# Kernel tuning notes

Hardware: AMD Instinct MI355X
Metric: run time of the kernel (lower is better)

Reference implementation:

```python
import jax, jax.numpy as jnp
import numpy as np

N_NODES = 100000
N_EDGES = 1600000
IN_F = 64
H1_F = 64
N_CLS = 16
NEG_SLOPE = 0.01  # F.leaky_relu default


def _sage_pool(x, src, dst, n_nodes, W_pool, b_pool, W_self, W_neigh, bias):
    """DGL SAGEConv with aggregator_type='pool'.
    msg = relu(x[src] @ W_pool + b_pool); pooled = max over in-edges per dst
    out = x @ W_self + pooled @ W_neigh + bias (empty segments pooled to 0)."""
    m = jax.nn.relu(x[src] @ W_pool + b_pool)                 # [E, d_in]
    pooled = jax.ops.segment_max(m, dst, num_segments=n_nodes)  # [N, d_in]
    deg = jax.ops.segment_sum(jnp.ones(dst.shape[0], x.dtype), dst,
                              num_segments=n_nodes)           # [N]
    pooled = jnp.where(deg[:, None] > 0, pooled, jnp.zeros((), x.dtype))
    return x @ W_self + pooled @ W_neigh + bias               # [N, d_out]


def setup_inputs() -> dict:
    key = jax.random.key(0)
    ks = jax.random.split(key, 12)
    sc_in = 1.0 / np.sqrt(IN_F)
    sc_h1 = 1.0 / np.sqrt(H1_F)
    inp = {
        "in_feat": jax.random.normal(ks[0], (N_NODES, IN_F), jnp.float32),
        "src": jax.random.randint(ks[1], (N_EDGES,), 0, N_NODES),
        "dst": jax.random.randint(ks[2], (N_EDGES,), 0, N_NODES),
        # layer 1 (in=64 -> out=64)
        "W_pool1": jax.random.normal(ks[3], (IN_F, IN_F), jnp.float32) * sc_in,
        "b_pool1": jnp.zeros((IN_F,), jnp.float32),
        "W_self1": jax.random.normal(ks[4], (IN_F, H1_F), jnp.float32) * sc_in,
        "W_neigh1": jax.random.normal(ks[5], (IN_F, H1_F), jnp.float32) * sc_in,
        "bias1": jnp.zeros((H1_F,), jnp.float32),
        # layer 2 (in=64 -> out=16)
        "W_pool2": jax.random.normal(ks[6], (H1_F, H1_F), jnp.float32) * sc_h1,
        "b_pool2": jnp.zeros((H1_F,), jnp.float32),
        "W_self2": jax.random.normal(ks[7], (H1_F, N_CLS), jnp.float32) * sc_h1,
        "W_neigh2": jax.random.normal(ks[8], (H1_F, N_CLS), jnp.float32) * sc_h1,
        "bias2": jnp.zeros((N_CLS,), jnp.float32),
    }
    return inp


def reference(in_feat, src, dst,
              W_pool1, b_pool1, W_self1, W_neigh1, bias1,
              W_pool2, b_pool2, W_self2, W_neigh2, bias2):
    n = in_feat.shape[0]
    h = _sage_pool(in_feat, src, dst, n, W_pool1, b_pool1, W_self1, W_neigh1, bias1)
    h = jnp.where(h >= 0, h, NEG_SLOPE * h)  # leaky_relu
    out = _sage_pool(h, src, dst, n, W_pool2, b_pool2, W_self2, W_neigh2, bias2)
    return out
```

## Files before the change

### kernel.cpp

```cpp
#include <hip/hip_runtime.h>
#include <cstddef>
#include <cstdint>

#define CAP 64
#define SCAP 40
#define CHUNK2 4096
#define PR 5120

typedef _Float16 h2 __attribute__((ext_vector_type(2)));
static __device__ __forceinline__ h2 h2max(h2 a, h2 b) {
  return __builtin_elementwise_max(a, b);
}
static __device__ __forceinline__ h2 bch2(int u) { return __builtin_bit_cast(h2, u); }
static __device__ __forceinline__ int packrelu(float a, float b) {
  h2 t; t.x = (_Float16)fmaxf(a, 0.f); t.y = (_Float16)fmaxf(b, 0.f);
  return __builtin_bit_cast(int, t);
}
static __device__ __forceinline__ int packleaky(float a, float b) {
  float la = (a >= 0.f) ? a : 0.01f * a;
  float lb = (b >= 0.f) ? b : 0.01f * b;
  h2 t; t.x = (_Float16)la; t.y = (_Float16)lb;
  return __builtin_bit_cast(int, t);
}
static __device__ __forceinline__ float fdot2f(h2 a, h2 b, float c) {
#if __has_builtin(__builtin_amdgcn_fdot2)
  return __builtin_amdgcn_fdot2(a, b, c, false);
#else
  return c + (float)a.x * (float)b.x + (float)a.y * (float)b.y;
#endif
}

__global__ __launch_bounds__(256) void k_binscatter(const int* __restrict__ src,
                                                    const int* __restrict__ dst,
                                                    unsigned int* __restrict__ pairs,
                                                    int* __restrict__ cnt2,
                                                    int E, int P) {
  __shared__ int hcnt[512];
  int tid = threadIdx.x;
  for (int p = tid; p < 512; p += 256) hcnt[p] = 0;
  __syncthreads();
  int chunk = blockIdx.x;
  int e0 = chunk * CHUNK2;
  unsigned int* pbase = pairs + (size_t)chunk * P * SCAP;
  #pragma unroll
  for (int k = 0; k < CHUNK2 / 256; k++) {
    int e = e0 + k * 256 + tid;
    if (e < E) {
      int d = dst[e], s = src[e];
      int p = d >> 8;
      int slot = atomicAdd(&hcnt[p], 1);
      if (slot < SCAP)
        pbase[p * SCAP + slot] = (unsigned)s | ((unsigned)(d & 255) << 17);
    }
  }
  __syncthreads();
  int* cbase = cnt2 + (size_t)chunk * P;
  for (int p = tid; p < P; p += 256) {
    int c = hcnt[p];
    cbase[p] = (c < SCAP) ? c : SCAP;
  }
}

__global__ __launch_bounds__(256) void k_fill3(const unsigned int* __restrict__ pairs,
                                               const int* __restrict__ cnt2,
                                               int* __restrict__ cnt,
                                               int* __restrict__ rowstart,
                                               int* __restrict__ bucket,
                                               int n, int NC, int P) {
  __shared__ int sbucket[256 * CAP];
  __shared__ int scnt[256];
  __shared__ int soff[256];
  __shared__ int scnt2[512];
  int tid = threadIdx.x;
  int p = blockIdx.x;
  scnt[tid] = 0;
  for (int c = tid; c < NC; c += 256) scnt2[c] = cnt2[(size_t)c * P + p];
  __syncthreads();
  int total = NC * SCAP;
  for (int t = tid; t < total; t += 256) {
    int chunk = t / SCAP;
    int slot = t - chunk * SCAP;
    if (slot < scnt2[chunk]) {
      unsigned int u = pairs[(size_t)chunk * P * SCAP + p * SCAP + slot];
      int s = (int)(u & 0x1FFFFu);
      int dlow = (int)(u >> 17);
      int sl = atomicAdd(&scnt[dlow], 1);
      if (sl < CAP)
        sbucket[dlow * CAP + sl] = s;
    }
  }
  __syncthreads();
  int c = scnt[tid];
  if (c > CAP) c = CAP;
  int ca = (c + 3) & ~3;
  soff[tid] = ca;
  __syncthreads();
  #pragma unroll
  for (int off = 1; off < 256; off <<= 1) {
    int t = (tid >= off) ? soff[tid - off] : 0;
    __syncthreads();
    soff[tid] += t;
    __syncthreads();
  }
  int local = soff[tid] - ca;
  int node = (p << 8) + tid;
  int gbase = p * PR + local;
  if (node < n) {
    cnt[node] = c;
    rowstart[node] = gbase;
  }
  for (int j = 0; j < c; j += 4) {
    int4 v = *(const int4*)&sbucket[tid * CAP + j];
    *(int4*)&bucket[gbase + j] = v;
  }
}

__global__ __launch_bounds__(256) void k_z(const float* __restrict__ X,
                                           const float* __restrict__ W,
                                           const float* __restrict__ bias,
                                           _Float16* __restrict__ Z, int n) {
  __shared__ __attribute__((aligned(16))) h2 sW[32 * 64];
  __shared__ __attribute__((aligned(16))) h2 sXT[32 * 128];
  int tid = threadIdx.x;
  #pragma unroll
  for (int it = 0; it < 8; it++) {
    int idx = it * 256 + tid;
    int kp = idx >> 6, c = idx & 63;
    h2 t;
    t.x = (_Float16)W[(2 * kp) * 64 + c];
    t.y = (_Float16)W[(2 * kp + 1) * 64 + c];
    sW[kp * 64 + c] = t;
  }
  int node0 = blockIdx.x * 128;
  #pragma unroll
  for (int it = 0; it < 8; it++) {
    int idx = it * 256 + tid;
    int row = idx & 127, c4 = idx >> 7;
    int node = node0 + row;
    float4 v = make_float4(0.f, 0.f, 0.f, 0.f);
    if (node < n) v = ((const float4*)(X + (size_t)node * 64))[c4];
    h2 a; a.x = (_Float16)v.x; a.y = (_Float16)v.y;
    h2 d; d.x = (_Float16)v.z; d.y = (_Float16)v.w;
    sXT[(2 * c4 + 0) * 128 + row] = a;
    sXT[(2 * c4 + 1) * 128 + row] = d;
  }
  __syncthreads();
  int lane = tid & 63;
  int cg = tid >> 6;
  float acc0[16], acc1[16];
  #pragma unroll
  for (int c4 = 0; c4 < 4; c4++) {
    float4 bv = ((const float4*)bias)[cg * 4 + c4];
    acc0[c4 * 4 + 0] = bv.x; acc0[c4 * 4 + 1] = bv.y;
    acc0[c4 * 4 + 2] = bv.z; acc0[c4 * 4 + 3] = bv.w;
    acc1[c4 * 4 + 0] = bv.x; acc1[c4 * 4 + 1] = bv.y;
    acc1[c4 * 4 + 2] = bv.z; acc1[c4 * 4 + 3] = bv.w;
  }
  #pragma unroll 8
  for (int kp = 0; kp < 32; kp++) {
    h2 x0 = sXT[kp * 128 + lane];
    h2 x1 = sXT[kp * 128 + lane + 64];
    const int4* wq = (const int4*)(sW + kp * 64 + cg * 16);
    #pragma unroll
    for (int q4 = 0; q4 < 4; q4++) {
      int4 wv = wq[q4];
      h2 w0 = bch2(wv.x), w1 = bch2(wv.y), w2 = bch2(wv.z), w3 = bch2(wv.w);
      acc0[q4 * 4 + 0] = fdot2f(x0, w0, acc0[q4 * 4 + 0]);
      acc0[q4 * 4 + 1] = fdot2f(x0, w1, acc0[q4 * 4 + 1]);
      acc0[q4 * 4 + 2] = fdot2f(x0, w2, acc0[q4 * 4 + 2]);
      acc0[q4 * 4 + 3] = fdot2f(x0, w3, acc0[q4 * 4 + 3]);
      acc1[q4 * 4 + 0] = fdot2f(x1, w0, acc1[q4 * 4 + 0]);
      acc1[q4 * 4 + 1] = fdot2f(x1, w1, acc1[q4 * 4 + 1]);
      acc1[q4 * 4 + 2] = fdot2f(x1, w2, acc1[q4 * 4 + 2]);
      acc1[q4 * 4 + 3] = fdot2f(x1, w3, acc1[q4 * 4 + 3]);
    }
  }
  int nodeA = node0 + lane;
  int nodeB = node0 + lane + 64;
  if (nodeA < n) {
    int4 o0, o1;
    o0.x = packrelu(acc0[0], acc0[1]);   o0.y = packrelu(acc0[2], acc0[3]);
    o0.z = packrelu(acc0[4], acc0[5]);   o0.w = packrelu(acc0[6], acc0[7]);
    o1.x = packrelu(acc0[8], acc0[9]);   o1.y = packrelu(acc0[10], acc0[11]);
    o1.z = packrelu(acc0[12], acc0[13]); o1.w = packrelu(acc0[14], acc0[15]);
    char* rp = (char*)Z + (size_t)nodeA * 128 + cg * 32;
    ((int4*)rp)[0] = o0; ((int4*)rp)[1] = o1;
  }
  if (nodeB < n) {
    int4 o0, o1;
    o0.x = packrelu(acc1[0], acc1[1]);   o0.y = packrelu(acc1[2], acc1[3]);
    o0.z = packrelu(acc1[4], acc1[5]);   o0.w = packrelu(acc1[6], acc1[7]);
    o1.x = packrelu(acc1[8], acc1[9]);   o1.y = packrelu(acc1[10], acc1[11]);
    o1.z = packrelu(acc1[12], acc1[13]); o1.w = packrelu(acc1[14], acc1[15]);
    char* rp = (char*)Z + (size_t)nodeB * 128 + cg * 32;
    ((int4*)rp)[0] = o0; ((int4*)rp)[1] = o1;
  }
}

__global__ __launch_bounds__(256) void k_hl(const float* __restrict__ X,
                                            const _Float16* __restrict__ P,
                                            const float* __restrict__ Ws,
                                            const float* __restrict__ Wn,
                                            const float* __restrict__ bias,
                                            const float* __restrict__ Wp2,
                                            const float* __restrict__ bp2,
                                            _Float16* __restrict__ H,
                                            _Float16* __restrict__ Z2, int n) {
  __shared__ __attribute__((aligned(16))) h2 sWs[32 * 64];
  __shared__ __attribute__((aligned(16))) h2 sWn[32 * 64];
  __shared__ __attribute__((aligned(16))) h2 sXT[32 * 128];
  __shared__ __attribute__((aligned(16))) h2 sPT[32 * 128];
  int tid = threadIdx.x;
  #pragma unroll
  for (int it = 0; it < 8; it++) {
    int idx = it * 256 + tid;
    int kp = idx >> 6, c = idx & 63;
    h2 t1, t2;
    t1.x = (_Float16)Ws[(2 * kp) * 64 + c];
    t1.y = (_Float16)Ws[(2 * kp + 1) * 64 + c];
    t2.x = (_Float16)Wn[(2 * kp) * 64 + c];
    t2.y = (_Float16)Wn[(2 * kp + 1) * 64 + c];
    sWs[kp * 64 + c] = t1;
    sWn[kp * 64 + c] = t2;
  }
  int node0 = blockIdx.x * 128;
  #pragma unroll
  for (int it = 0; it < 8; it++) {
    int idx = it * 256 + tid;
    int row = idx & 127, c4 = idx >> 7;
    int node = node0 + row;
    float4 v = make_float4(0.f, 0.f, 0.f, 0.f);
    if (node < n) v = ((const float4*)(X + (size_t)node * 64))[c4];
    h2 a; a.x = (_Float16)v.x; a.y = (_Float16)v.y;
    h2 d; d.x = (_Float16)v.z; d.y = (_Float16)v.w;
    sXT[(2 * c4 + 0) * 128 + row] = a;
    sXT[(2 * c4 + 1) * 128 + row] = d;
  }
  #pragma unroll
  for (int it = 0; it < 4; it++) {
    int idx = it * 256 + tid;
    int row = idx & 127, q = idx >> 7;
    int node = node0 + row;
    int4 u = make_int4(0, 0, 0, 0);
    if (node < n) u = ((const int4*)((const char*)P + (size_t)node * 128))[q];
    sPT[(4 * q + 0) * 128 + row] = bch2(u.x);
    sPT[(4 * q + 1) * 128 + row] = bch2(u.y);
    sPT[(4 * q + 2) * 128 + row] = bch2(u.z);
    sPT[(4 * q + 3) * 128 + row] = bch2(u.w);
  }
  __syncthreads();
  int lane = tid & 63;
  int cg = tid >> 6;
  float acc0[16], acc1[16];
  #pragma unroll
  for (int c4 = 0; c4 < 4; c4++) {
    float4 bv = ((const float4*)bias)[cg * 4 + c4];
    acc0[c4 * 4 + 0] = bv.x; acc0[c4 * 4 + 1] = bv.y;
    acc0[c4 * 4 + 2] = bv.z; acc0[c4 * 4 + 3] = bv.w;
    acc1[c4 * 4 + 0] = bv.x; acc1[c4 * 4 + 1] = bv.y;
    acc1[c4 * 4 + 2] = bv.z; acc1[c4 * 4 + 3] = bv.w;
  }
  #pragma unroll 8
  for (int kp = 0; kp < 32; kp++) {
    h2 x0 = sXT[kp * 128 + lane];
    h2 x1 = sXT[kp * 128 + lane + 64];
    h2 p0 = sPT[kp * 128 + lane];
    h2 p1 = sPT[kp * 128 + lane + 64];
    const int4* wsq = (const int4*)(sWs + kp * 64 + cg * 16);
    const int4* wnq = (const int4*)(sWn + kp * 64 + cg * 16);
    #pragma unroll
    for (int q4 = 0; q4 < 4; q4++) {
      int4 a = wsq[q4];
      int4 d = wnq[q4];
      h2 s0 = bch2(a.x), s1 = bch2(a.y), s2 = bch2(a.z), s3 = bch2(a.w);
      h2 n0 = bch2(d.x), n1 = bch2(d.y), n2 = bch2(d.z), n3 = bch2(d.w);
      acc0[q4 * 4 + 0] = fdot2f(x0, s0, acc0[q4 * 4 + 0]);
      acc0[q4 * 4 + 1] = fdot2f(x0, s1, acc0[q4 * 4 + 1]);
      acc0[q4 * 4 + 2] = fdot2f(x0, s2, acc0[q4 * 4 + 2]);
      acc0[q4 * 4 + 3] = fdot2f(x0, s3, acc0[q4 * 4 + 3]);
      acc0[q4 * 4 + 0] = fdot2f(p0, n0, acc0[q4 * 4 + 0]);
      acc0[q4 * 4 + 1] = fdot2f(p0, n1, acc0[q4 * 4 + 1]);
      acc0[q4 * 4 + 2] = fdot2f(p0, n2, acc0[q4 * 4 + 2]);
      acc0[q4 * 4 + 3] = fdot2f(p0, n3, acc0[q4 * 4 + 3]);
      acc1[q4 * 4 + 0] = fdot2f(x1, s0, acc1[q4 * 4 + 0]);
      acc1[q4 * 4 + 1] = fdot2f(x1, s1, acc1[q4 * 4 + 1]);
      acc1[q4 * 4 + 2] = fdot2f(x1, s2, acc1[q4 * 4 + 2]);
      acc1[q4 * 4 + 3] = fdot2f(x1, s3, acc1[q4 * 4 + 3]);
      acc1[q4 * 4 + 0] = fdot2f(p1, n0, acc1[q4 * 4 + 0]);
      acc1[q4 * 4 + 1] = fdot2f(p1, n1, acc1[q4 * 4 + 1]);
      acc1[q4 * 4 + 2] = fdot2f(p1, n2, acc1[q4 * 4 + 2]);
      acc1[q4 * 4 + 3] = fdot2f(p1, n3, acc1[q4 * 4 + 3]);
    }
  }
  int ha[8], hb[8];
  #pragma unroll
  for (int j = 0; j < 8; j++) {
    ha[j] = packleaky(acc0[2 * j], acc0[2 * j + 1]);
    hb[j] = packleaky(acc1[2 * j], acc1[2 * j + 1]);
  }
  int nodeA = node0 + lane;
  int nodeB = node0 + lane + 64;
  __syncthreads();
  #pragma unroll
  for (int j = 0; j < 8; j++) {
    sXT[(cg * 8 + j) * 128 + lane]      = bch2(ha[j]);
    sXT[(cg * 8 + j) * 128 + lane + 64] = bch2(hb[j]);
  }
  #pragma unroll
  for (int it = 0; it < 8; it++) {
    int idx = it * 256 + tid;
    int kp = idx >> 6, c = idx & 63;
    h2 t;
    t.x = (_Float16)Wp2[(2 * kp) * 64 + c];
    t.y = (_Float16)Wp2[(2 * kp + 1) * 64 + c];
    sWs[kp * 64 + c] = t;
  }
  if (nodeA < n) {
    char* rp = (char*)H + (size_t)nodeA * 128 + cg * 32;
    ((int4*)rp)[0] = make_int4(ha[0], ha[1], ha[2], ha[3]);
    ((int4*)rp)[1] = make_int4(ha[4], ha[5], ha[6], ha[7]);
  }
  if (nodeB < n) {
    char* rp = (char*)H + (size_t)nodeB * 128 + cg * 32;
    ((int4*)rp)[0] = make_int4(hb[0], hb[1], hb[2], hb[3]);
    ((int4*)rp)[1] = make_int4(hb[4], hb[5], hb[6], hb[7]);
  }
  __syncthreads();
  float c0[16], c1[16];
  #pragma unroll
  for (int c4 = 0; c4 < 4; c4++) {
    float4 bv = ((const float4*)bp2)[cg * 4 + c4];
    c0[c4 * 4 + 0] = bv.x; c0[c4 * 4 + 1] = bv.y;
    c0[c4 * 4 + 2] = bv.z; c0[c4 * 4 + 3] = bv.w;
    c1[c4 * 4 + 0] = bv.x; c1[c4 * 4 + 1] = bv.y;
    c1[c4 * 4 + 2] = bv.z; c1[c4 * 4 + 3] = bv.w;
  }
  #pragma unroll 8
  for (int kp = 0; kp < 32; kp++) {
    h2 x0 = sXT[kp * 128 + lane];
    h2 x1 = sXT[kp * 128 + lane + 64];
    const int4* wq = (const int4*)(sWs + kp * 64 + cg * 16);
    #pragma unroll
    for (int q4 = 0; q4 < 4; q4++) {
      int4 wv = wq[q4];
      h2 w0 = bch2(wv.x), w1 = bch2(wv.y), w2 = bch2(wv.z), w3 = bch2(wv.w);
      c0[q4 * 4 + 0] = fdot2f(x0, w0, c0[q4 * 4 + 0]);
      c0[q4 * 4 + 1] = fdot2f(x0, w1, c0[q4 * 4 + 1]);
      c0[q4 * 4 + 2] = fdot2f(x0, w2, c0[q4 * 4 + 2]);
      c0[q4 * 4 + 3] = fdot2f(x0, w3, c0[q4 * 4 + 3]);
      c1[q4 * 4 + 0] = fdot2f(x1, w0, c1[q4 * 4 + 0]);
      c1[q4 * 4 + 1] = fdot2f(x1, w1, c1[q4 * 4 + 1]);
      c1[q4 * 4 + 2] = fdot2f(x1, w2, c1[q4 * 4 + 2]);
      c1[q4 * 4 + 3] = fdot2f(x1, w3, c1[q4 * 4 + 3]);
    }
  }
  if (nodeA < n) {
    int4 o0, o1;
    o0.x = packrelu(c0[0], c0[1]);   o0.y = packrelu(c0[2], c0[3]);
    o0.z = packrelu(c0[4], c0[5]);   o0.w = packrelu(c0[6], c0[7]);
    o1.x = packrelu(c0[8], c0[9]);   o1.y = packrelu(c0[10], c0[11]);
    o1.z = packrelu(c0[12], c0[13]); o1.w = packrelu(c0[14], c0[15]);
    char* rp = (char*)Z2 + (size_t)nodeA * 128 + cg * 32;
    ((int4*)rp)[0] = o0; ((int4*)rp)[1] = o1;
  }
  if (nodeB < n) {
    int4 o0, o1;
    o0.x = packrelu(c1[0], c1[1]);   o0.y = packrelu(c1[2], c1[3]);
    o0.z = packrelu(c1[4], c1[5]);   o0.w = packrelu(c1[6], c1[7]);
    o1.x = packrelu(c1[8], c1[9]);   o1.y = packrelu(c1[10], c1[11]);
    o1.z = packrelu(c1[12], c1[13]); o1.w = packrelu(c1[14], c1[15]);
    char* rp = (char*)Z2 + (size_t)nodeB * 128 + cg * 32;
    ((int4*)rp)[0] = o0; ((int4*)rp)[1] = o1;
  }
}

__global__ __launch_bounds__(256) void k_gather(const _Float16* __restrict__ Z,
                                                const int* __restrict__ bucket,
                                                const int* __restrict__ rowstart,
                                                const int* __restrict__ cnt,
                                                _Float16* __restrict__ pooled, int n) {
  int t = blockIdx.x * 256 + threadIdx.x;
  int node = t >> 5;
  int sub = t & 31;
  if (node >= n) return;
  int c = cnt[node];
  const int* bk = bucket + rowstart[node];
  const char* zb = (const char*)Z + sub * 4;
  h2 acc = (h2)(_Float16)0;
  int j = 0;
  for (; j + 8 <= c; j += 8) {
    int4 a = *(const int4*)(bk + j);
    int4 d = *(const int4*)(bk + j + 4);
    int u0 = *(const int*)(zb + (size_t)a.x * 128);
    int u1 = *(const int*)(zb + (size_t)a.y * 128);
    int u2 = *(const int*)(zb + (size_t)a.z * 128);
    int u3 = *(const int*)(zb + (size_t)a.w * 128);
    int u4 = *(const int*)(zb + (size_t)d.x * 128);
    int u5 = *(const int*)(zb + (size_t)d.y * 128);
    int u6 = *(const int*)(zb + (size_t)d.z * 128);
    int u7 = *(const int*)(zb + (size_t)d.w * 128);
    h2 m0 = h2max(bch2(u0), bch2(u1));
    h2 m1 = h2max(bch2(u2), bch2(u3));
    h2 m2 = h2max(bch2(u4), bch2(u5));
    h2 m3 = h2max(bch2(u6), bch2(u7));
    acc = h2max(acc, h2max(h2max(m0, m1), h2max(m2, m3)));
  }
  if (j + 4 <= c) {
    int4 a = *(const int4*)(bk + j);
    int u0 = *(const int*)(zb + (size_t)a.x * 128);
    int u1 = *(const int*)(zb + (size_t)a.y * 128);
    int u2 = *(const int*)(zb + (size_t)a.z * 128);
    int u3 = *(const int*)(zb + (size_t)a.w * 128);
    acc = h2max(acc, h2max(h2max(bch2(u0), bch2(u1)), h2max(bch2(u2), bch2(u3))));
    j += 4;
  }
  if (j + 2 <= c) {
    int2 a = *(const int2*)(bk + j);
    int u0 = *(const int*)(zb + (size_t)a.x * 128);
    int u1 = *(const int*)(zb + (size_t)a.y * 128);
    acc = h2max(acc, h2max(bch2(u0), bch2(u1)));
    j += 2;
  }
  if (j < c) {
    int u0 = *(const int*)(zb + (size_t)bk[j] * 128);
    acc = h2max(acc, bch2(u0));
  }
  *(int*)((char*)pooled + (size_t)node * 128 + sub * 4) = __builtin_bit_cast(int, acc);
}

__global__ __launch_bounds__(256) void k_gather_out(const _Float16* __restrict__ Z,
                                                    const int* __restrict__ bucket,
                                                    const int* __restrict__ rowstart,
                                                    const int* __restrict__ cnt,
                                                    const _Float16* __restrict__ Hrow,
                                                    const float* __restrict__ Ws,
                                                    const float* __restrict__ Wn,
                                                    const float* __restrict__ bias,
                                                    float* __restrict__ OUT, int n) {
  __shared__ __attribute__((aligned(16))) h2 sWs[32 * 16];
  __shared__ __attribute__((aligned(16))) h2 sWn[32 * 16];
  __shared__ __attribute__((aligned(16))) h2 sH[8][32];
  __shared__ __attribute__((aligned(16))) h2 sP[8][32];
  __shared__ float sB[16];
  int tid = threadIdx.x;
  #pragma unroll
  for (int it = 0; it < 2; it++) {
    int idx = it * 256 + tid;
    int kp = idx >> 4, c = idx & 15;
    h2 t1, t2;
    t1.x = (_Float16)Ws[(2 * kp) * 16 + c];
    t1.y = (_Float16)Ws[(2 * kp + 1) * 16 + c];
    t2.x = (_Float16)Wn[(2 * kp) * 16 + c];
    t2.y = (_Float16)Wn[(2 * kp + 1) * 16 + c];
    sWs[kp * 16 + c] = t1;
    sWn[kp * 16 + c] = t2;
  }
  if (tid < 16) sB[tid] = bias[tid];
  int nodeBase = blockIdx.x * 8;
  if (tid < 64) {
    int nd = nodeBase + (tid >> 3);
    int q = tid & 7;
    int4 u = make_int4(0, 0, 0, 0);
    if (nd < n) u = ((const int4*)((const char*)Hrow + (size_t)nd * 128))[q];
    ((int4*)&sH[tid >> 3][0])[q] = u;
  }
  int en = tid >> 5;
  int node = nodeBase + en;
  int sub = tid & 31;
  h2 acc = (h2)(_Float16)0;
  if (node < n) {
    int c = cnt[node];
    const int* bk = bucket + rowstart[node];
    const char* zb = (const char*)Z + sub * 4;
    int j = 0;
    for (; j + 8 <= c; j += 8) {
      int4 a = *(const int4*)(bk + j);
      int4 d = *(const int4*)(bk + j + 4);
      int u0 = *(const int*)(zb + (size_t)a.x * 128);
      int u1 = *(const int*)(zb + (size_t)a.y * 128);
      int u2 = *(const int*)(zb + (size_t)a.z * 128);
      int u3 = *(const int*)(zb + (size_t)a.w * 128);
      int u4 = *(const int*)(zb + (size_t)d.x * 128);
      int u5 = *(const int*)(zb + (size_t)d.y * 128);
      int u6 = *(const int*)(zb + (size_t)d.z * 128);
      int u7 = *(const int*)(zb + (size_t)d.w * 128);
      h2 m0 = h2max(bch2(u0), bch2(u1));
      h2 m1 = h2max(bch2(u2), bch2(u3));
      h2 m2 = h2max(bch2(u4), bch2(u5));
      h2 m3 = h2max(bch2(u6), bch2(u7));
      acc = h2max(acc, h2max(h2max(m0, m1), h2max(m2, m3)));
    }
    if (j + 4 <= c) {
      int4 a = *(const int4*)(bk + j);
      int u0 = *(const int*)(zb + (size_t)a.x * 128);
      int u1 = *(const int*)(zb + (size_t)a.y * 128);
      int u2 = *(const int*)(zb + (size_t)a.z * 128);
      int u3 = *(const int*)(zb + (size_t)a.w * 128);
      acc = h2max(acc, h2max(h2max(bch2(u0), bch2(u1)), h2max(bch2(u2), bch2(u3))));
      j += 4;
    }
    if (j + 2 <= c) {
      int2 a = *(const int2*)(bk + j);
      int u0 = *(const int*)(zb + (size_t)a.x * 128);
      int u1 = *(const int*)(zb + (size_t)a.y * 128);
      acc = h2max(acc, h2max(bch2(u0), bch2(u1)));
      j += 2;
    }
    if (j < c) {
      int u0 = *(const int*)(zb + (size_t)bk[j] * 128);
      acc = h2max(acc, bch2(u0));
    }
  }
  sP[en][sub] = acc;
  __syncthreads();
  int col = tid & 15;
  int kh = (tid >> 4) & 1;
  float v = 0.f;
  #pragma unroll
  for (int j = 0; j < 16; j++) {
    int kp = kh * 16 + j;
    v = fdot2f(sH[en][kp], sWs[kp * 16 + col], v);
    v = fdot2f(sP[en][kp], sWn[kp * 16 + col], v);
  }
  v += __shfl_xor(v, 16);
  if (kh == 0 && node < n)
    OUT[(size_t)node * 16 + col] = v + sB[col];
}

extern "C" void kernel_launch(void* const* d_in, const int* in_sizes, int n_in,
                              void* d_out, int out_size, void* d_ws, size_t ws_size,
                              hipStream_t stream) {
  const float* X   = (const float*)d_in[0];
  const int*   src = (const int*)d_in[1];
  const int*   dst = (const int*)d_in[2];
  const float* Wp1 = (const float*)d_in[3];
  const float* bp1 = (const float*)d_in[4];
  const float* Ws1 = (const float*)d_in[5];
  const float* Wn1 = (const float*)d_in[6];
  const float* b1  = (const float*)d_in[7];
  const float* Wp2 = (const float*)d_in[8];
  const float* bp2 = (const float*)d_in[9];
  const float* Ws2 = (const float*)d_in[10];
  const float* Wn2 = (const float*)d_in[11];
  const float* b2  = (const float*)d_in[12];
  float* OUT = (float*)d_out;

  const int n = in_sizes[0] / 64;
  const int E = in_sizes[1];
  const int P = (n + 255) >> 8;
  const int NC = (E + CHUNK2 - 1) / CHUNK2;

  char* w = (char*)d_ws;
  auto alloc = [&](size_t bytes) -> char* {
    char* p = w;
    w += (bytes + 255) & ~(size_t)255;
    return p;
  };
  int*  cnt      = (int*)alloc((size_t)n * 4);
  int*  rowstart = (int*)alloc((size_t)n * 4);
  int*  bucket   = (int*)alloc((size_t)P * PR * 4);
  int*  cnt2     = (int*)alloc((size_t)NC * P * 4);
  size_t pairs_b = (size_t)NC * P * SCAP * 4;
  size_t h_b     = (size_t)n * 64 * 2;
  char* ali = alloc(pairs_b > h_b ? pairs_b : h_b);
  unsigned int* pairs = (unsigned int*)ali;
  _Float16*     h16   = (_Float16*)ali;
  _Float16* zh     = (_Float16*)alloc((size_t)n * 64 * 2);
  _Float16* pooled = (_Float16*)alloc((size_t)n * 64 * 2);
  (void)ws_size; (void)n_in; (void)out_size;

  const int nbT  = (n + 127) / 128;
  const int nbG  = (n * 32 + 255) / 256;
  const int nbG8 = (n + 7) / 8;

  k_binscatter<<<NC, 256, 0, stream>>>(src, dst, pairs, cnt2, E, P);
  k_fill3<<<P, 256, 0, stream>>>(pairs, cnt2, cnt, rowstart, bucket, n, NC, P);

  k_z<<<nbT, 256, 0, stream>>>(X, Wp1, bp1, zh, n);
  k_gather<<<nbG, 256, 0, stream>>>(zh, bucket, rowstart, cnt, pooled, n);
  k_hl<<<nbT, 256, 0, stream>>>(X, pooled, Ws1, Wn1, b1, Wp2, bp2, h16, zh, n);
  k_gather_out<<<nbG8, 256, 0, stream>>>(zh, bucket, rowstart, cnt, h16,
                                         Ws2, Wn2, b2, OUT, n);
}
```

Before: 190.5 us.

## Merge binscatter with Z projection and pack row count into offset

The edge bin-scatter and the layer-1 pool projection now run as one launch, with the block index choosing the role, so the two independent stages overlap and one launch is saved. Row start and degree are packed into a single int, so each gather reads one index word instead of two. The layer-1 gather now handles two nodes per 32-lane group to give each thread more memory-level parallelism. PR is enlarged to leave room for the packed offset, at the cost of a larger bucket buffer and a 10-bit count field.

Result: faster. 180.4 us (-5.3%).

```diff
diff --git a/kernel.cpp b/kernel.cpp
--- a/kernel.cpp
+++ b/kernel.cpp
@@ -5,7 +5,7 @@
 #define CAP 64
 #define SCAP 40
 #define CHUNK2 4096
-#define PR 5120
+#define PR 5632
 
 typedef _Float16 h2 __attribute__((ext_vector_type(2)));
 static __device__ __forceinline__ h2 h2max(h2 a, h2 b) {
@@ -30,98 +30,45 @@
 #endif
 }
 
-__global__ __launch_bounds__(256) void k_binscatter(const int* __restrict__ src,
-                                                    const int* __restrict__ dst,
-                                                    unsigned int* __restrict__ pairs,
-                                                    int* __restrict__ cnt2,
-                                                    int E, int P) {
-  __shared__ int hcnt[512];
+__global__ __launch_bounds__(256) void k_build(const int* __restrict__ src,
+                                               const int* __restrict__ dst,
+                                               unsigned int* __restrict__ pairs,
+                                               int* __restrict__ cnt2,
+                                               int E, int P, int NC,
+                                               const float* __restrict__ X,
+                                               const float* __restrict__ W,
+                                               const float* __restrict__ bias,
+                                               _Float16* __restrict__ Z, int n) {
+  __shared__ __attribute__((aligned(16))) char smem[24576];
   int tid = threadIdx.x;
-  for (int p = tid; p < 512; p += 256) hcnt[p] = 0;
-  __syncthreads();
-  int chunk = blockIdx.x;
-  int e0 = chunk * CHUNK2;
-  unsigned int* pbase = pairs + (size_t)chunk * P * SCAP;
-  #pragma unroll
-  for (int k = 0; k < CHUNK2 / 256; k++) {
-    int e = e0 + k * 256 + tid;
-    if (e < E) {
-      int d = dst[e], s = src[e];
-      int p = d >> 8;
-      int slot = atomicAdd(&hcnt[p], 1);
-      if (slot < SCAP)
-        pbase[p * SCAP + slot] = (unsigned)s | ((unsigned)(d & 255) << 17);
+  if ((int)blockIdx.x < NC) {
+    int* hcnt = (int*)smem;
+    for (int p = tid; p < 512; p += 256) hcnt[p] = 0;
+    __syncthreads();
+    int chunk = blockIdx.x;
+    int e0 = chunk * CHUNK2;
+    unsigned int* pbase = pairs + (size_t)chunk * P * SCAP;
+    #pragma unroll
+    for (int k = 0; k < CHUNK2 / 256; k++) {
+      int e = e0 + k * 256 + tid;
+      if (e < E) {
+        int d = dst[e], s = src[e];
+        int p = d >> 8;
+        int slot = atomicAdd(&hcnt[p], 1);
+        if (slot < SCAP)
+          pbase[p * SCAP + slot] = (unsigned)s | ((unsigned)(d & 255) << 17);
+      }
     }
-  }
-  __syncthreads();
-  int* cbase = cnt2 + (size_t)chunk * P;
-  for (int p = tid; p < P; p += 256) {
-    int c = hcnt[p];
-    cbase[p] = (c < SCAP) ? c : SCAP;
-  }
-}
-
-__global__ __launch_bounds__(256) void k_fill3(const unsigned int* __restrict__ pairs,
-                                               const int* __restrict__ cnt2,
-                                               int* __restrict__ cnt,
-                                               int* __restrict__ rowstart,
-                                               int* __restrict__ bucket,
-                                               int n, int NC, int P) {
-  __shared__ int sbucket[256 * CAP];
-  __shared__ int scnt[256];
-  __shared__ int soff[256];
-  __shared__ int scnt2[512];
-  int tid = threadIdx.x;
-  int p = blockIdx.x;
-  scnt[tid] = 0;
-  for (int c = tid; c < NC; c += 256) scnt2[c] = cnt2[(size_t)c * P + p];
-  __syncthreads();
-  int total = NC * SCAP;
-  for (int t = tid; t < total; t += 256) {
-    int chunk = t / SCAP;
-    int slot = t - chunk * SCAP;
-    if (slot < scnt2[chunk]) {
-      unsigned int u = pairs[(size_t)chunk * P * SCAP + p * SCAP + slot];
-      int s = (int)(u & 0x1FFFFu);
-      int dlow = (int)(u >> 17);
-      int sl = atomicAdd(&scnt[dlow], 1);
-      if (sl < CAP)
-        sbucket[dlow * CAP + sl] = s;
+    __syncthreads();
+    int* cbase = cnt2 + (size_t)chunk * P;
+    for (int p = tid; p < P; p += 256) {
+      int c = hcnt[p];
+      cbase[p] = (c < SCAP) ? c : SCAP;
     }
-  }
-  __syncthreads();
-  int c = scnt[tid];
-  if (c > CAP) c = CAP;
-  int ca = (c + 3) & ~3;
-  soff[tid] = ca;
-  __syncthreads();
-  #pragma unroll
-  for (int off = 1; off < 256; off <<= 1) {
-    int t = (tid >= off) ? soff[tid - off] : 0;
-    __syncthreads();
-    soff[tid] += t;
-    __syncthreads();
-  }
-  int local = soff[tid] - ca;
-  int node = (p << 8) + tid;
-  int gbase = p * PR + local;
-  if (node < n) {
-    cnt[node] = c;
-    rowstart[node] = gbase;
-  }
-  for (int j = 0; j < c; j += 4) {
-    int4 v = *(const int4*)&sbucket[tid * CAP + j];
-    *(int4*)&bucket[gbase + j] = v;
-  }
-}
-
-__global__ __launch_bounds__(256) void k_z(const float* __restrict__ X,
-                                           const float* __restrict__ W,
-                                           const float* __restrict__ bias,
-                                           _Float16* __restrict__ Z, int n) {
-  __shared__ __attribute__((aligned(16))) h2 sW[32 * 64];
-  __shared__ __attribute__((aligned(16))) h2 sXT[32 * 128];
-  int tid = threadIdx.x;
+    return;
+  }
+  h2* sW  = (h2*)smem;
+  h2* sXT = (h2*)(smem + 8192);
   #pragma unroll
   for (int it = 0; it < 8; it++) {
     int idx = it * 256 + tid;
@@ -131,7 +78,7 @@
     t.y = (_Float16)W[(2 * kp + 1) * 64 + c];
     sW[kp * 64 + c] = t;
   }
-  int node0 = blockIdx.x * 128;
+  int node0 = (blockIdx.x - NC) * 128;
   #pragma unroll
   for (int it = 0; it < 8; it++) {
     int idx = it * 256 + tid;
@@ -194,6 +141,129 @@
     o1.z = packrelu(acc1[12], acc1[13]); o1.w = packrelu(acc1[14], acc1[15]);
     char* rp = (char*)Z + (size_t)nodeB * 128 + cg * 32;
     ((int4*)rp)[0] = o0; ((int4*)rp)[1] = o1;
+  }
+}
+
+__global__ __launch_bounds__(256) void k_fill3(const unsigned int* __restrict__ pairs,
+                                               const int* __restrict__ cnt2,
+                                               int* __restrict__ rowcnt,
+                                               int* __restrict__ bucket,
+                                               int n, int NC, int P) {
+  __shared__ int sbucket[256 * CAP];
+  __shared__ int scnt[256];
+  __shared__ int soff[256];
+  __shared__ int scnt2[512];
+  int tid = threadIdx.x;
+  int p = blockIdx.x;
+  scnt[tid] = 0;
+  for (int c = tid; c < NC; c += 256) scnt2[c] = cnt2[(size_t)c * P + p];
+  __syncthreads();
+  int total = NC * SCAP;
+  for (int t = tid; t < total; t += 256) {
+    int chunk = t / SCAP;
+    int slot = t - chunk * SCAP;
+    if (slot < scnt2[chunk]) {
+      unsigned int u = pairs[(size_t)chunk * P * SCAP + p * SCAP + slot];
+      int s = (int)(u & 0x1FFFFu);
+      int dlow = (int)(u >> 17);
+      int sl = atomicAdd(&scnt[dlow], 1);
+      if (sl < CAP)
+        sbucket[dlow * CAP + sl] = s;
+    }
+  }
+  __syncthreads();
+  int c = scnt[tid];
+  if (c > CAP) c = CAP;
+  int ca = (c + 3) & ~3;
+  soff[tid] = ca;
+  __syncthreads();
+  #pragma unroll
+  for (int off = 1; off < 256; off <<= 1) {
+    int t = (tid >= off) ? soff[tid - off] : 0;
+    __syncthreads();
+    soff[tid] += t;
+    __syncthreads();
+  }
+  int local = soff[tid] - ca;
+  int node = (p << 8) + tid;
+  int gbase = p * PR + local;
+  if (node < n)
+    rowcnt[node] = gbase | (c << 22);
+  for (int j = 0; j < c; j += 4) {
+    int4 v = *(const int4*)&sbucket[tid * CAP + j];
+    *(int4*)&bucket[gbase + j] = v;
+  }
+}
+
+static __device__ __forceinline__ h2 gather_one(const char* zb,
+                                                const int* __restrict__ bucket,
+                                                int rc) {
+  int c = rc >> 22;
+  const int* bk = bucket + (rc & 0x3FFFFF);
+  h2 acc = (h2)(_Float16)0;
+  int j = 0;
+  for (; j + 8 <= c; j += 8) {
+    int4 a = *(const int4*)(bk + j);
+    int4 d = *(const int4*)(bk + j + 4);
+    int u0 = *(const int*)(zb + (size_t)a.x * 128);
+    int u1 = *(const int*)(zb + (size_t)a.y * 128);
+    int u2 = *(const int*)(zb + (size_t)a.z * 128);
+    int u3 = *(const int*)(zb + (size_t)a.w * 128);
+    int u4 = *(const int*)(zb + (size_t)d.x * 128);
+    int u5 = *(const int*)(zb + (size_t)d.y * 128);
+    int u6 = *(const int*)(zb + (size_t)d.z * 128);
+    int u7 = *(const int*)(zb + (size_t)d.w * 128);
+    h2 m0 = h2max(bch2(u0), bch2(u1));
+    h2 m1 = h2max(bch2(u2), bch2(u3));
+    h2 m2 = h2max(bch2(u4), bch2(u5));
+    h2 m3 = h2max(bch2(u6), bch2(u7));
+    acc = h2max(acc, h2max(h2max(m0, m1), h2max(m2, m3)));
+  }
+  if (j + 4 <= c) {
+    int4 a = *(const int4*)(bk + j);
+    int u0 = *(const int*)(zb + (size_t)a.x * 128);
+    int u1 = *(const int*)(zb + (size_t)a.y * 128);
+    int u2 = *(const int*)(zb + (size_t)a.z * 128);
+    int u3 = *(const int*)(zb + (size_t)a.w * 128);
+    acc = h2max(acc, h2max(h2max(bch2(u0), bch2(u1)), h2max(bch2(u2), bch2(u3))));
+    j += 4;
+  }
+  if (j + 2 <= c) {
+    int2 a = *(const int2*)(bk + j);
+    int u0 = *(const int*)(zb + (size_t)a.x * 128);
+    int u1 = *(const int*)(zb + (size_t)a.y * 128);
+    acc = h2max(acc, h2max(bch2(u0), bch2(u1)));
+    j += 2;
+  }
+  if (j < c) {
+    int u0 = *(const int*)(zb + (size_t)bk[j] * 128);
+    acc = h2max(acc, bch2(u0));
+  }
+  return acc;
+}
+
+__global__ __launch_bounds__(256) void k_gather2(const _Float16* __restrict__ Z,
+                                                 const int* __restrict__ bucket,
+                                                 const int* __restrict__ rowcnt,
+                                                 _Float16* __restrict__ pooled, int n) {
+  int t = blockIdx.x * 256 + threadIdx.x;
+  int pairid = t >> 5;
+  int sub = t & 31;
+  int nA = pairid * 2;
+  int nB = nA + 1;
+  if (nA >= n) return;
+  const char* zb = (const char*)Z + sub * 4;
+  int rcA = rowcnt[nA];
+  h2 accA, accB;
+  if (nB < n) {
+    int rcB = rowcnt[nB];
+    accA = gather_one(zb, bucket, rcA);
+    accB = gather_one(zb, bucket, rcB);
+    *(int*)((char*)pooled + (size_t)nA * 128 + sub * 4) = __builtin_bit_cast(int, accA);
+    *(int*)((char*)pooled + (size_t)nB * 128 + sub * 4) = __builtin_bit_cast(int, accB);
+  } else {
+    accA = gather_one(zb, bucket, rcA);
+    *(int*)((char*)pooled + (size_t)nA * 128 + sub * 4) = __builtin_bit_cast(int, accA);
   }
 }
 
@@ -374,64 +444,9 @@
   }
 }
 
-__global__ __launch_bounds__(256) void k_gather(const _Float16* __restrict__ Z,
-                                                const int* __restrict__ bucket,
-                                                const int* __restrict__ rowstart,
-                                                const int* __restrict__ cnt,
-                                                _Float16* __restrict__ pooled, int n) {
-  int t = blockIdx.x * 256 + threadIdx.x;
-  int node = t >> 5;
-  int sub = t & 31;
-  if (node >= n) return;
-  int c = cnt[node];
-  const int* bk = bucket + rowstart[node];
-  const char* zb = (const char*)Z + sub * 4;
-  h2 acc = (h2)(_Float16)0;
-  int j = 0;
-  for (; j + 8 <= c; j += 8) {
-    int4 a = *(const int4*)(bk + j);
-    int4 d = *(const int4*)(bk + j + 4);
-    int u0 = *(const int*)(zb + (size_t)a.x * 128);
-    int u1 = *(const int*)(zb + (size_t)a.y * 128);
-    int u2 = *(const int*)(zb + (size_t)a.z * 128);
-    int u3 = *(const int*)(zb + (size_t)a.w * 128);
-    int u4 = *(const int*)(zb + (size_t)d.x * 128);
-    int u5 = *(const int*)(zb + (size_t)d.y * 128);
-    int u6 = *(const int*)(zb + (size_t)d.z * 128);
-    int u7 = *(const int*)(zb + (size_t)d.w * 128);
-    h2 m0 = h2max(bch2(u0), bch2(u1));
-    h2 m1 = h2max(bch2(u2), bch2(u3));
-    h2 m2 = h2max(bch2(u4), bch2(u5));
-    h2 m3 = h2max(bch2(u6), bch2(u7));
-    acc = h2max(acc, h2max(h2max(m0, m1), h2max(m2, m3)));
-  }
-  if (j + 4 <= c) {
-    int4 a = *(const int4*)(bk + j);
-    int u0 = *(const int*)(zb + (size_t)a.x * 128);
-    int u1 = *(const int*)(zb + (size_t)a.y * 128);
-    int u2 = *(const int*)(zb + (size_t)a.z * 128);
-    int u3 = *(const int*)(zb + (size_t)a.w * 128);
-    acc = h2max(acc, h2max(h2max(bch2(u0), bch2(u1)), h2max(bch2(u2), bch2(u3))));
-    j += 4;
-  }
-  if (j + 2 <= c) {
-    int2 a = *(const int2*)(bk + j);
-    int u0 = *(const int*)(zb + (size_t)a.x * 128);
-    int u1 = *(const int*)(zb + (size_t)a.y * 128);
-    acc = h2max(acc, h2max(bch2(u0), bch2(u1)));
-    j += 2;
-  }
-  if (j < c) {
-    int u0 = *(const int*)(zb + (size_t)bk[j] * 128);
-    acc = h2max(acc, bch2(u0));
-  }
-  *(int*)((char*)pooled + (size_t)node * 128 + sub * 4) = __builtin_bit_cast(int, acc);
-}
-
 __global__ __launch_bounds__(256) void k_gather_out(const _Float16* __restrict__ Z,
                                                     const int* __restrict__ bucket,
-                                                    const int* __restrict__ rowstart,
-                                                    const int* __restrict__ cnt,
+                                                    const int* __restrict__ rowcnt,
                                                     const _Float16* __restrict__ Hrow,
                                                     const float* __restrict__ Ws,
                                                     const float* __restrict__ Wn,
@@ -468,49 +483,8 @@
   int node = nodeBase + en;
   int sub = tid & 31;
   h2 acc = (h2)(_Float16)0;
-  if (node < n) {
-    int c = cnt[node];
-    const int* bk = bucket + rowstart[node];
-    const char* zb = (const char*)Z + sub * 4;
-    int j = 0;
-    for (; j + 8 <= c; j += 8) {
-      int4 a = *(const int4*)(bk + j);
-      int4 d = *(const int4*)(bk + j + 4);
-      int u0 = *(const int*)(zb + (size_t)a.x * 128);
-      int u1 = *(const int*)(zb + (size_t)a.y * 128);
-      int u2 = *(const int*)(zb + (size_t)a.z * 128);
-      int u3 = *(const int*)(zb + (size_t)a.w * 128);
-      int u4 = *(const int*)(zb + (size_t)d.x * 128);
-      int u5 = *(const int*)(zb + (size_t)d.y * 128);
-      int u6 = *(const int*)(zb + (size_t)d.z * 128);
-      int u7 = *(const int*)(zb + (size_t)d.w * 128);
-      h2 m0 = h2max(bch2(u0), bch2(u1));
-      h2 m1 = h2max(bch2(u2), bch2(u3));
-      h2 m2 = h2max(bch2(u4), bch2(u5));
-      h2 m3 = h2max(bch2(u6), bch2(u7));
-      acc = h2max(acc, h2max(h2max(m0, m1), h2max(m2, m3)));
-    }
-    if (j + 4 <= c) {
-      int4 a = *(const int4*)(bk + j);
-      int u0 = *(const int*)(zb + (size_t)a.x * 128);
-      int u1 = *(const int*)(zb + (size_t)a.y * 128);
-      int u2 = *(const int*)(zb + (size_t)a.z * 128);
-      int u3 = *(const int*)(zb + (size_t)a.w * 128);
-      acc = h2max(acc, h2max(h2max(bch2(u0), bch2(u1)), h2max(bch2(u2), bch2(u3))));
-      j += 4;
-    }
-    if (j + 2 <= c) {
-      int2 a = *(const int2*)(bk + j);
-      int u0 = *(const int*)(zb + (size_t)a.x * 128);
-      int u1 = *(const int*)(zb + (size_t)a.y * 128);
-      acc = h2max(acc, h2max(bch2(u0), bch2(u1)));
-      j += 2;
-    }
-    if (j < c) {
-      int u0 = *(const int*)(zb + (size_t)bk[j] * 128);
-      acc = h2max(acc, bch2(u0));
-    }
-  }
+  if (node < n)
+    acc = gather_one((const char*)Z + sub * 4, bucket, rowcnt[node]);
   sP[en][sub] = acc;
   __syncthreads();
   int col = tid & 15;
@@ -556,10 +530,9 @@
     w += (bytes + 255) & ~(size_t)255;
     return p;
   };
-  int*  cnt      = (int*)alloc((size_t)n * 4);
-  int*  rowstart = (int*)alloc((size_t)n * 4);
-  int*  bucket   = (int*)alloc((size_t)P * PR * 4);
-  int*  cnt2     = (int*)alloc((size_t)NC * P * 4);
+  int*  rowcnt = (int*)alloc((size_t)n * 4);
+  int*  bucket = (int*)alloc((size_t)P * PR * 4);
+  int*  cnt2   = (int*)alloc((size_t)NC * P * 4);
   size_t pairs_b = (size_t)NC * P * SCAP * 4;
   size_t h_b     = (size_t)n * 64 * 2;
   char* ali = alloc(pairs_b > h_b ? pairs_b : h_b);
@@ -570,15 +543,14 @@
   (void)ws_size; (void)n_in; (void)out_size;
 
   const int nbT  = (n + 127) / 128;
-  const int nbG  = (n * 32 + 255) / 256;
+  const int nbG2 = (n * 16 + 255) / 256;
   const int nbG8 = (n + 7) / 8;
 
-  k_binscatter<<<NC, 256, 0, stream>>>(src, dst, pairs, cnt2, E, P);
-  k_fill3<<<P, 256, 0, stream>>>(pairs, cnt2, cnt, rowstart, bucket, n, NC, P);
-
-  k_z<<<nbT, 256, 0, stream>>>(X, Wp1, bp1, zh, n);
-  k_gather<<<nbG, 256, 0, stream>>>(zh, bucket, rowstart, cnt, pooled, n);
+  k_build<<<NC + nbT, 256, 0, stream>>>(src, dst, pairs, cnt2, E, P, NC,
+                                        X, Wp1, bp1, zh, n);
+  k_fill3<<<P, 256, 0, stream>>>(pairs, cnt2, rowcnt, bucket, n, NC, P);
+  k_gather2<<<nbG2, 256, 0, stream>>>(zh, bucket, rowcnt, pooled, n);
   k_hl<<<nbT, 256, 0, stream>>>(X, pooled, Ws1, Wn1, b1, Wp2, bp2, h16, zh, n);
-  k_gather_out<<<nbG8, 256, 0, stream>>>(zh, bucket, rowstart, cnt, h16,
+  k_gather_out<<<nbG8, 256, 0, stream>>>(zh, bucket, rowcnt, h16,
                                          Ws2, Wn2, b2, OUT, n);
 }
```
